# Kernel optimization log

Hardware: AMD Instinct MI355X
Metric: run time of the kernel (lower is better)

Reference implementation:

```python
import jax, jax.numpy as jnp
import numpy as np

B, T, C, H, R = 4, 2048, 1024, 16, 64
D = C // H  # head_dim = 64
ALPHA = 0.7  # init_alpha; alpha_proj is None so c_proj also uses 0.7


def _harmonic_linear(x, U, V):
    # W = U @ diag(s) @ V with harmonic decay s_k = (k+1)^{-alpha}; y = x @ W^T
    s = (jnp.arange(R, dtype=x.dtype) + 1.0) ** (-ALPHA)
    return ((x @ V.T) * s) @ U.T


def setup_inputs() -> dict:
    key = jax.random.key(0)
    ks = jax.random.split(key, 9)
    p = lambda k, shape: 0.02 * jax.random.normal(k, shape, dtype=jnp.float32)
    return {
        "x": jax.random.normal(ks[0], (B, T, C), dtype=jnp.float32),
        "q_U": p(ks[1], (C, R)), "q_V": p(ks[2], (R, C)),
        "k_U": p(ks[3], (C, R)), "k_V": p(ks[4], (R, C)),
        "v_U": p(ks[5], (C, R)), "v_V": p(ks[6], (R, C)),
        "c_U": p(ks[7], (C, R)), "c_V": p(ks[8], (R, C)),
    }


def reference(x, q_U, q_V, k_U, k_V, v_U, v_V, c_U, c_V):
    # projections -> [B, H, T, D]
    def split_heads(t):
        return t.reshape(B, T, H, D).transpose(0, 2, 1, 3)

    q = split_heads(_harmonic_linear(x, q_U, q_V))
    k = split_heads(_harmonic_linear(x, k_U, k_V))
    v = split_heads(_harmonic_linear(x, v_U, v_V))

    scale = 1.0 / np.sqrt(D).astype(np.float32)
    att = jnp.einsum("bhqd,bhkd->bhqk", q, k) * scale  # [B,H,T,T]
    causal = jnp.tril(jnp.ones((T, T), dtype=bool))
    att = jnp.where(causal[None, None], att, jnp.finfo(att.dtype).min)
    att = jax.nn.softmax(att, axis=-1)  # dropout p=0.0 -> identity

    y = jnp.einsum("bhqk,bhkd->bhqd", att, v)  # [B,H,T,D]
    y = y.transpose(0, 2, 1, 3).reshape(B, T, C)
    return _harmonic_linear(y, c_U, c_V)
```

## Files before the change

### kernel.cpp

```cpp
#include <hip/hip_runtime.h>
#include <hip/hip_bf16.h>
#include <math.h>


#define NB 4
#define NT 2048
#define NC 1024
#define NH 16
#define NR 64
#define ND 64
#define NM (NB * NT)

typedef __attribute__((ext_vector_type(8))) short short8;
typedef __attribute__((ext_vector_type(4))) short short4v;
typedef __attribute__((ext_vector_type(4))) float f32x4;
typedef __attribute__((ext_vector_type(4))) float float4v;
typedef __attribute__((ext_vector_type(4))) int int4v;

__device__ __forceinline__ short f2bf(float f) {
    union { __hip_bfloat16 h; short s; } u;
    u.h = __float2bfloat16(f);
    return u.s;
}
__device__ __forceinline__ float bf2f(short s) {
    union { short s; __hip_bfloat16 h; } u;
    u.s = s;
    return __bfloat162float(u.h);
}
__device__ __forceinline__ f32x4 MFMA(short8 a, short8 b, f32x4 c) {
    return __builtin_amdgcn_mfma_f32_16x16x32_bf16(a, b, c, 0, 0, 0);
}
__device__ __forceinline__ float exp2_(float x) {
#if __has_builtin(__builtin_amdgcn_exp2f)
    return __builtin_amdgcn_exp2f(x);
#else
    return exp2f(x);
#endif
}

typedef const __attribute__((address_space(1))) unsigned int* gas_ptr;
typedef __attribute__((address_space(3))) unsigned int* las_ptr;
__device__ __forceinline__ void gll16(const void* g, void* l) {
    __builtin_amdgcn_global_load_lds((gas_ptr)g, (las_ptr)l, 16, 0, 0);
}

__global__ __launch_bounds__(256) void k_prep(const float* __restrict__ qV, const float* __restrict__ kV,
                                              const float* __restrict__ vV, const float* __restrict__ cV,
                                              const float* __restrict__ qU, const float* __restrict__ kU,
                                              const float* __restrict__ vU, const float* __restrict__ cU,
                                              short* __restrict__ Whi, short* __restrict__ Wlo) {
    const int idx = blockIdx.x * 256 + threadIdx.x;
    const int mat = idx >> 13;
    const int f = idx & 8191;
    const int l = f & 63;
    const int rest = f >> 6;
    const float* src;
    switch (mat) {
        case 0: src = qV; break;
        case 1: src = kV; break;
        case 2: src = vV; break;
        case 3: src = cV; break;
        case 4: src = qU; break;
        case 5: src = kU; break;
        case 6: src = vU; break;
        default: src = cU; break;
    }
    int row, col, stride;
    if (mat < 4) {
        const int s = rest & 31, nt = rest >> 5;
        row = nt * 16 + (l & 15);
        col = s * 32 + (l >> 4) * 8;
        stride = NC;
    } else {
        const int ks = rest & 1, tn = rest >> 1;
        row = tn * 16 + (l & 15);
        col = ks * 32 + (l >> 4) * 8;
        stride = NR;
    }
    float sc = 1.0f;
    if (mat < 4) sc = powf((float)(row + 1), -0.7f);
    if (mat == 4) sc = 0.125f * 1.44269504088896f;
    const float* p = src + (size_t)row * stride + col;
    const float4v a = *(const float4v*)p;
    const float4v b = *(const float4v*)(p + 4);
    float v[8] = {a[0], a[1], a[2], a[3], b[0], b[1], b[2], b[3]};
    short* oh = Whi + (size_t)mat * 65536 + (size_t)f * 8;
    short* ol = Wlo + (size_t)mat * 65536 + (size_t)f * 8;
    short4v h0, h1, l0, l1;
#pragma unroll
    for (int j = 0; j < 8; j++) {
        const float fv = v[j] * sc;
        const short h = f2bf(fv);
        const short lo = f2bf(fv - bf2f(h));
        if (j < 4) { h0[j] = h; l0[j] = lo; } else { h1[j - 4] = h; l1[j - 4] = lo; }
    }
    *(short4v*)oh = h0;
    *(short4v*)(oh + 4) = h1;
    *(short4v*)ol = l0;
    *(short4v*)(ol + 4) = l1;
}

__global__ __launch_bounds__(512, 2) void k_qkv(const float* __restrict__ X,
                                                const short* __restrict__ Whi, const short* __restrict__ Wlo,
                                                short* __restrict__ qb, short* __restrict__ kb,
                                                short* __restrict__ vtb) {
    __shared__ __align__(16) char Xl[2][16384];
    __shared__ __align__(16) short Thi[32 * 200];
    __shared__ __align__(16) short Tlov[32 * 72];
    const int tid = threadIdx.x;
    const int w = tid >> 6, l = tid & 63;
    const int lr = l & 15, lk = l >> 4;
    const int g = w & 3, mg = w >> 2;
    const int mb = blockIdx.x * 32;

    auto stageX = [&](int buf, int win) {
#pragma unroll
        for (int q = 0; q < 2; q++) {
            const int r = q * 16 + w * 2 + (l >> 5);
            const int c = l & 31;
            const int sc16 = c ^ (r & 15);
            const float* gp = X + (size_t)(mb + r) * NC + win * 128 + sc16 * 4;
            gll16(gp, (char*)Xl[buf] + q * 8192 + w * 1024);
        }
    };

    const short* Wqk_f = (g < 2) ? Whi : (Whi + 65536);
    const int tA = ((g & 1) * 2) * 32;
    const int tB = tA + 32;
    const int tV = g * 32;
    const short* vfh = Whi + 2 * 65536;
    const short* vfl = Wlo + 2 * 65536;

    f32x4 a0 = 0.0f, a1 = 0.0f, av = 0.0f;
    const int xrow = (mg * 16 + lr) * 512;
    stageX(0, 0);
    for (int win = 0; win < 8; ++win) {
        const int buf = win & 1;
        __syncthreads();
        if (win < 7) stageX(buf ^ 1, win + 1);
        const char* XB = Xl[buf];
#pragma unroll
        for (int kk = 0; kk < 4; ++kk) {
            const int cb = kk * 8 + lk * 2;
            const float4v xa = *(const float4v*)(XB + xrow + ((cb ^ lr) << 4));
            const float4v xb = *(const float4v*)(XB + xrow + (((cb + 1) ^ lr) << 4));
            float xv[8] = {xa[0], xa[1], xa[2], xa[3], xb[0], xb[1], xb[2], xb[3]};
            short8 xh, xl8;
#pragma unroll
            for (int jj = 0; jj < 8; jj++) {
                const short h = f2bf(xv[jj]);
                xh[jj] = h;
                xl8[jj] = f2bf(xv[jj] - bf2f(h));
            }
            const int s = win * 4 + kk;
            const short8 wa = *(const short8*)(Wqk_f + (size_t)((tA + s) * 64 + l) * 8);
            const short8 wb = *(const short8*)(Wqk_f + (size_t)((tB + s) * 64 + l) * 8);
            const short8 wvh = *(const short8*)(vfh + (size_t)((tV + s) * 64 + l) * 8);
            const short8 wvl = *(const short8*)(vfl + (size_t)((tV + s) * 64 + l) * 8);
            a0 = MFMA(xh, wa, a0);
            a1 = MFMA(xh, wb, a1);
            av = MFMA(xh, wvh, av);
            av = MFMA(xh, wvl, av);
            av = MFMA(xl8, wvh, av);
        }
    }
    {
        const int p = g >> 1;
        const int colA = p * 64 + (g & 1) * 32 + lr;
        const int colB = colA + 16;
        const int colV = 128 + g * 16 + lr;
#pragma unroll
        for (int i = 0; i < 4; i++) {
            const int row = mg * 16 + lk * 4 + i;
            Thi[row * 200 + colA] = f2bf(a0[i]);
            Thi[row * 200 + colB] = f2bf(a1[i]);
            const short hv = f2bf(av[i]);
            Thi[row * 200 + colV] = hv;
            Tlov[row * 72 + g * 16 + lr] = f2bf(av[i] - bf2f(hv));
        }
    }
    __syncthreads();
    const short* qUf = Whi + 4 * 65536;
    const short* kUf = Whi + 5 * 65536;
    const short* vUfh = Whi + 6 * 65536;
    const short* vUfl = Wlo + 6 * 65536;
    short8 tf[2][3][2];
    short8 tfl[2][2];
#pragma unroll
    for (int m2 = 0; m2 < 2; m2++) {
        const int trow = m2 * 16 + lr;
#pragma unroll
        for (int ks = 0; ks < 2; ks++) {
#pragma unroll
            for (int p = 0; p < 3; p++)
                tf[m2][p][ks] = *(const short8*)(Thi + trow * 200 + p * 64 + ks * 32 + lk * 8);
            tfl[m2][ks] = *(const short8*)(Tlov + trow * 72 + ks * 32 + lk * 8);
        }
    }
    const int bb = mb >> 11, mt = mb & (NT - 1);
#pragma unroll 2
    for (int nt = 0; nt < 8; nt++) {
        const int tn = w * 8 + nt;
        short8 uq[2], uk[2], uvh[2], uvl[2];
#pragma unroll
        for (int ks = 0; ks < 2; ks++) {
            const size_t off2 = (size_t)((tn * 2 + ks) * 64 + l) * 8;
            uq[ks] = *(const short8*)(qUf + off2);
            uk[ks] = *(const short8*)(kUf + off2);
            uvh[ks] = *(const short8*)(vUfh + off2);
            uvl[ks] = *(const short8*)(vUfl + off2);
        }
#pragma unroll
        for (int m2 = 0; m2 < 2; m2++) {
            f32x4 aq = 0.0f, ak = 0.0f, avv = 0.0f;
#pragma unroll
            for (int ks = 0; ks < 2; ks++) {
                aq = MFMA(uq[ks], tf[m2][0][ks], aq);
                ak = MFMA(uk[ks], tf[m2][1][ks], ak);
                avv = MFMA(tf[m2][2][ks], uvh[ks], avv);
                avv = MFMA(tf[m2][2][ks], uvl[ks], avv);
                avv = MFMA(tfl[m2][ks], uvh[ks], avv);
            }
            const int tt = mt + m2 * 16 + lr;
            const int nq = tn * 16 + lk * 4;
            const int hhq = nq >> 6, ddq = nq & 63;
            short4v pq, pk;
#pragma unroll
            for (int i = 0; i < 4; i++) { pq[i] = f2bf(aq[i]); pk[i] = f2bf(ak[i]); }
            *(short4v*)(qb + ((size_t)(bb * NH + hhq) * NT + tt) * ND + ddq) = pq;
            *(short4v*)(kb + ((size_t)(bb * NH + hhq) * NT + tt) * ND + ddq) = pk;
            const int n = tn * 16 + lr;
            const int hhv = n >> 6, ddv = n & 63;
            const int tv = mt + m2 * 16 + lk * 4;
            short4v pv;
#pragma unroll
            for (int i = 0; i < 4; i++) pv[i] = f2bf(avv[i]);
            *(short4v*)(vtb + ((size_t)(bb * NH + hhv) * ND + ddv) * NT + tv) = pv;
        }
    }
}

__global__ __launch_bounds__(512, 2) void k_cout(const short* __restrict__ Yb,
                                                 const short* __restrict__ Whi, const short* __restrict__ Wlo,
                                                 float* __restrict__ Out) {
    __shared__ __align__(16) char Yl[2][16384];
    __shared__ __align__(16) short tyhi[32 * 72];
    __shared__ __align__(16) short tylo[32 * 72];
    const int tid = threadIdx.x;
    const int w = tid >> 6, l = tid & 63;
    const int lr = l & 15, lk = l >> 4;
    const int g = w & 3, mg = w >> 2;
    const int mb = blockIdx.x * 32;
    const short* cVfh = Whi + 3 * 65536;
    const short* cVfl = Wlo + 3 * 65536;
    const short* cUfh = Whi + 7 * 65536;
    const short* cUfl = Wlo + 7 * 65536;

    auto stageY = [&](int buf, int win) {
#pragma unroll
        for (int q = 0; q < 2; q++) {
            const int r = q * 16 + w * 2 + (l >> 5);
            const int c = l & 31;
            const int sc16 = c ^ (r & 15);
            const short* gp = Yb + (size_t)(mb + r) * NC + win * 256 + sc16 * 8;
            gll16(gp, (char*)Yl[buf] + q * 8192 + w * 1024);
        }
    };

    const int tV = g * 32;
    f32x4 acc = 0.0f;
    const int xrow = (mg * 16 + lr) * 512;
    stageY(0, 0);
    for (int win = 0; win < 4; ++win) {
        const int buf = win & 1;
        __syncthreads();
        if (win < 3) stageY(buf ^ 1, win + 1);
        const char* YB = Yl[buf];
#pragma unroll
        for (int kk = 0; kk < 8; ++kk) {
            const short8 ah = *(const short8*)(YB + xrow + ((((kk * 4 + lk)) ^ lr) << 4));
            const int s = win * 8 + kk;
            const short8 wh = *(const short8*)(cVfh + (size_t)((tV + s) * 64 + l) * 8);
            const short8 wl = *(const short8*)(cVfl + (size_t)((tV + s) * 64 + l) * 8);
            acc = MFMA(ah, wh, acc);
            acc = MFMA(ah, wl, acc);
        }
    }
#pragma unroll
    for (int i = 0; i < 4; i++) {
        const int row = mg * 16 + lk * 4 + i;
        const short h = f2bf(acc[i]);
        tyhi[row * 72 + g * 16 + lr] = h;
        tylo[row * 72 + g * 16 + lr] = f2bf(acc[i] - bf2f(h));
    }
    __syncthreads();
    short8 th[2][2], tl[2][2];
#pragma unroll
    for (int m2 = 0; m2 < 2; m2++) {
        const int trow = m2 * 16 + lr;
#pragma unroll
        for (int ks = 0; ks < 2; ks++) {
            th[m2][ks] = *(const short8*)(tyhi + trow * 72 + ks * 32 + lk * 8);
            tl[m2][ks] = *(const short8*)(tylo + trow * 72 + ks * 32 + lk * 8);
        }
    }
#pragma unroll 2
    for (int nt = 0; nt < 8; nt++) {
        const int tn = w * 8 + nt;
        short8 uh[2], ul[2];
#pragma unroll
        for (int ks = 0; ks < 2; ks++) {
            const size_t off2 = (size_t)((tn * 2 + ks) * 64 + l) * 8;
            uh[ks] = *(const short8*)(cUfh + off2);
            ul[ks] = *(const short8*)(cUfl + off2);
        }
#pragma unroll
        for (int m2 = 0; m2 < 2; m2++) {
            f32x4 a = 0.0f;
#pragma unroll
            for (int ks = 0; ks < 2; ks++) {
                a = MFMA(uh[ks], th[m2][ks], a);
                a = MFMA(ul[ks], th[m2][ks], a);
                a = MFMA(uh[ks], tl[m2][ks], a);
            }
            const int mm = mb + m2 * 16 + lr;
            const int n = tn * 16 + lk * 4;
            *(float4v*)(Out + (size_t)mm * NC + n) = *(float4v*)&a;
        }
    }
}

__device__ __forceinline__ short8 lds_frag(const short* base, int row, int cb) {
    return *(const short8*)((const char*)base + (((row << 7) + cb) ^ ((row & 7) << 4)));
}

__global__ __launch_bounds__(256, 2) void k_attn(const short* __restrict__ Qm,
                                                 const short* __restrict__ Km,
                                                 const short* __restrict__ Vt,
                                                 short* __restrict__ Y) {
    __shared__ __align__(16) short Kl[2][64 * 64];
    __shared__ __align__(16) short Vl[2][64 * 64];
    __shared__ __align__(16) short Pl[8 * 1024];
    const int tid = threadIdx.x;
    const int w = tid >> 6, l = tid & 63;
    const int lr = l & 15, lk = l >> 4;
    const int lin = blockIdx.y * 8 + blockIdx.x;
    const int nl = (lin & 7) * 64 + (lin >> 3);
    const int j = nl & 7;
    const int bh = nl >> 3;
    const int ntile = 32 - 2 * j;
    const int qA0 = 128 * j + w * 32;
    const int qB0 = (1920 - 128 * j) + w * 32;
    const int diagA = 2 * j + (w >> 1);
    const int diagB = 30 - 2 * j + (w >> 1);

    const short* Kb = Km + (size_t)bh * NT * ND;
    const short* Vb = Vt + (size_t)bh * ND * NT;

    short8 qfA[2][2], qfB[2][2];
#pragma unroll
    for (int f = 0; f < 2; f++) {
#pragma unroll
        for (int ks = 0; ks < 2; ks++) {
            qfA[f][ks] = *(const short8*)(Qm + ((size_t)bh * NT + qA0 + f * 16 + lr) * ND + ks * 32 + lk * 8);
            qfB[f][ks] = *(const short8*)(Qm + ((size_t)bh * NT + qB0 + f * 16 + lr) * ND + ks * 32 + lk * 8);
        }
    }

    const int grow8 = w * 8 + (l >> 3);
    const int gcolb = (((l & 7) ^ ((l >> 3) & 7)) << 4);
    auto stage = [&](int buf, int kv0) {
        const char* kp = (const char*)Kb + (((size_t)(kv0 + grow8)) << 7) + gcolb;
        const char* vp = (const char*)Vb + (size_t)grow8 * (NT * 2) + kv0 * 2 + gcolb;
        char* kl = (char*)Kl[buf] + w * 1024;
        char* vl = (char*)Vl[buf] + w * 1024;
        gll16(kp, kl);
        gll16(kp + (32 << 7), kl + 4096);
        gll16(vp, vl);
        gll16(vp + (size_t)32 * NT * 2, vl + 4096);
    };

    f32x4 lsA[2], lsB[2];
    f32x4 oA[2][4], oB[2][4];
#pragma unroll
    for (int f = 0; f < 2; f++) {
        lsA[f] = 0.0f;
        lsB[f] = 0.0f;
#pragma unroll
        for (int dt = 0; dt < 4; dt++) { oA[f][dt] = 0.0f; oB[f][dt] = 0.0f; }
    }

    auto computeG = [&](const short8 (&qf)[2][2], f32x4 (&ls)[2], f32x4 (&o)[2][4],
                        const short* KlB, const short* VlB, bool diag) {
        f32x4 sa[2][4];
#pragma unroll
        for (int f = 0; f < 2; f++)
#pragma unroll
            for (int nt = 0; nt < 4; nt++) sa[f][nt] = -16.0f;
        __builtin_amdgcn_s_setprio(1);
#pragma unroll
        for (int ks = 0; ks < 2; ks++) {
#pragma unroll
            for (int nt = 0; nt < 4; nt++) {
                const short8 kf = lds_frag(KlB, nt * 16 + lr, ks * 64 + lk * 16);
                sa[0][nt] = MFMA(kf, qf[0][ks], sa[0][nt]);
                sa[1][nt] = MFMA(kf, qf[1][ks], sa[1][nt]);
            }
        }
        __builtin_amdgcn_s_setprio(0);
        if (diag) {
#pragma unroll
            for (int f = 0; f < 2; f++) {
                const int qrel = (w & 1) * 32 + f * 16 + lr;
#pragma unroll
                for (int nt = 0; nt < 4; nt++) {
                    const int kvb = nt * 16 + lk * 4;
#pragma unroll
                    for (int i = 0; i < 4; i++)
                        if (kvb + i > qrel) sa[f][nt][i] = -1e30f;
                }
            }
        }
#pragma unroll
        for (int f = 0; f < 2; f++) {
            char* plbf = (char*)Pl + w * 4096 + f * 2048;
#pragma unroll
            for (int nt = 0; nt < 4; nt++) {
                f32x4 sv;
#pragma unroll
                for (int i = 0; i < 4; i++) sv[i] = exp2_(sa[f][nt][i]);
                ls[f] += sv;
                short4v pk;
#pragma unroll
                for (int i = 0; i < 4; i++) pk[i] = f2bf(sv[i]);
                *(short4v*)(plbf + (((lr << 7) + ((nt * 16 + lk * 4) << 1)) ^ ((lr & 7) << 4))) = pk;
            }
        }
        short8 pb[2][2];
#pragma unroll
        for (int f = 0; f < 2; f++) {
            const char* plbf = (const char*)Pl + w * 4096 + f * 2048;
            pb[f][0] = *(const short8*)(plbf + (((lr << 7) + ((lk * 8) << 1)) ^ ((lr & 7) << 4)));
            pb[f][1] = *(const short8*)(plbf + (((lr << 7) + ((32 + lk * 8) << 1)) ^ ((lr & 7) << 4)));
        }
        __builtin_amdgcn_s_setprio(1);
#pragma unroll
        for (int ks = 0; ks < 2; ks++) {
#pragma unroll
            for (int dt = 0; dt < 4; dt++) {
                const short8 vf = lds_frag(VlB, dt * 16 + lr, ks * 64 + lk * 16);
                o[0][dt] = MFMA(vf, pb[0][ks], o[0][dt]);
                o[1][dt] = MFMA(vf, pb[1][ks], o[1][dt]);
            }
        }
        __builtin_amdgcn_s_setprio(0);
    };

    stage(0, 0);
    for (int it = 0; it < ntile; ++it) {
        const int buf = it & 1;
        __syncthreads();
        if (it + 1 < ntile) stage(buf ^ 1, (it + 1) * 64);
        const short* KlB = Kl[buf];
        const short* VlB = Vl[buf];
        if (it <= diagA) computeG(qfA, lsA, oA, KlB, VlB, it == diagA);
        if (it <= diagB) computeG(qfB, lsB, oB, KlB, VlB, it == diagB);
    }

    const int b = bh >> 4, h = bh & 15;
#pragma unroll
    for (int f = 0; f < 2; f++) {
        float lA = (lsA[f][0] + lsA[f][1]) + (lsA[f][2] + lsA[f][3]);
        float lB = (lsB[f][0] + lsB[f][1]) + (lsB[f][2] + lsB[f][3]);
        lA += __shfl_xor(lA, 16);
        lA += __shfl_xor(lA, 32);
        lB += __shfl_xor(lB, 16);
        lB += __shfl_xor(lB, 32);
        const float invA = 1.0f / lA, invB = 1.0f / lB;
        short* ypA = Y + ((size_t)b * NT + (qA0 + f * 16 + lr)) * NC + h * ND;
        short* ypB = Y + ((size_t)b * NT + (qB0 + f * 16 + lr)) * NC + h * ND;
#pragma unroll
        for (int dt = 0; dt < 4; dt++) {
            short4v ya, yb2;
#pragma unroll
            for (int i = 0; i < 4; i++) {
                ya[i] = f2bf(oA[f][dt][i] * invA);
                yb2[i] = f2bf(oB[f][dt][i] * invB);
            }
            *(short4v*)(ypA + dt * 16 + lk * 4) = ya;
            *(short4v*)(ypB + dt * 16 + lk * 4) = yb2;
        }
    }
}

extern "C" void kernel_launch(void* const* d_in, const int* in_sizes, int n_in,
                              void* d_out, int out_size, void* d_ws, size_t ws_size,
                              hipStream_t stream) {
    const float* x = (const float*)d_in[0];
    const float* qU = (const float*)d_in[1];
    const float* qV = (const float*)d_in[2];
    const float* kU = (const float*)d_in[3];
    const float* kV = (const float*)d_in[4];
    const float* vU = (const float*)d_in[5];
    const float* vV = (const float*)d_in[6];
    const float* cU = (const float*)d_in[7];
    const float* cV = (const float*)d_in[8];
    float* out = (float*)d_out;

    char* ws = (char*)d_ws;
    size_t off = 0;
    auto take = [&](size_t bytes) {
        char* p = ws + off;
        off += (bytes + 255) & ~(size_t)255;
        return p;
    };
    short* Whi = (short*)take(8 * 65536 * 2);
    short* Wlo = (short*)take(8 * 65536 * 2);
    short* qb = (short*)take((size_t)NM * NC * 2);
    short* kb = (short*)take((size_t)NM * NC * 2);
    short* vtb = (short*)take((size_t)NM * NC * 2);
    short* yb = (short*)take((size_t)NM * NC * 2);

    k_prep<<<256, 256, 0, stream>>>(qV, kV, vV, cV, qU, kU, vU, cU, Whi, Wlo);
    k_qkv<<<256, 512, 0, stream>>>(x, Whi, Wlo, qb, kb, vtb);
    k_attn<<<dim3(8, NB * NH), 256, 0, stream>>>(qb, kb, vtb, yb);
    k_cout<<<256, 512, 0, stream>>>(yb, Whi, Wlo, out);
}
```

Measured before the change: 117.8 us.

## Stage 128-key KV tiles and share K/V fragments across both query groups

Doubles the shared-memory K/V stage from 64 to 128 keys per barrier, halving the number of __syncthreads in the attention loop. The QK/softmax and PV stages are split so K and V fragments are read from LDS once per sub-tile into registers and reused by both query groups A and B, instead of being reloaded for each group. In exchange, LDS use per block roughly doubles and register pressure rises from the held K/V fragment arrays, which may reduce occupancy.

```diff
diff --git a/kernel.cpp b/kernel.cpp
--- a/kernel.cpp
+++ b/kernel.cpp
@@ -338,8 +338,8 @@
                                                  const short* __restrict__ Km,
                                                  const short* __restrict__ Vt,
                                                  short* __restrict__ Y) {
-    __shared__ __align__(16) short Kl[2][64 * 64];
-    __shared__ __align__(16) short Vl[2][64 * 64];
+    __shared__ __align__(16) short Kl[2][8192];
+    __shared__ __align__(16) short Vl[2][8192];
     __shared__ __align__(16) short Pl[8 * 1024];
     const int tid = threadIdx.x;
     const int w = tid >> 6, l = tid & 63;
@@ -349,6 +349,7 @@
     const int j = nl & 7;
     const int bh = nl >> 3;
     const int ntile = 32 - 2 * j;
+    const int np = 16 - j;
     const int qA0 = 128 * j + w * 32;
     const int qB0 = (1920 - 128 * j) + w * 32;
     const int diagA = 2 * j + (w >> 1);
@@ -369,15 +370,20 @@
 
     const int grow8 = w * 8 + (l >> 3);
     const int gcolb = (((l & 7) ^ ((l >> 3) & 7)) << 4);
-    auto stage = [&](int buf, int kv0) {
-        const char* kp = (const char*)Kb + (((size_t)(kv0 + grow8)) << 7) + gcolb;
-        const char* vp = (const char*)Vb + (size_t)grow8 * (NT * 2) + kv0 * 2 + gcolb;
+    auto stage2 = [&](int buf, int kv0) {
         char* kl = (char*)Kl[buf] + w * 1024;
         char* vl = (char*)Vl[buf] + w * 1024;
-        gll16(kp, kl);
-        gll16(kp + (32 << 7), kl + 4096);
-        gll16(vp, vl);
-        gll16(vp + (size_t)32 * NT * 2, vl + 4096);
+#pragma unroll
+        for (int c = 0; c < 4; ++c) {
+            const char* kp = (const char*)Kb + (((size_t)(kv0 + c * 32 + grow8)) << 7) + gcolb;
+            gll16(kp, kl + c * 4096);
+        }
+#pragma unroll
+        for (int c = 0; c < 4; ++c) {
+            const int tt = c >> 1, dh = c & 1;
+            const char* vp = (const char*)Vb + (size_t)(dh * 32 + grow8) * (NT * 2) + (kv0 + tt * 64) * 2 + gcolb;
+            gll16(vp, vl + tt * 8192 + dh * 4096);
+        }
     };
 
     f32x4 lsA[2], lsB[2];
@@ -390,8 +396,8 @@
         for (int dt = 0; dt < 4; dt++) { oA[f][dt] = 0.0f; oB[f][dt] = 0.0f; }
     }
 
-    auto computeG = [&](const short8 (&qf)[2][2], f32x4 (&ls)[2], f32x4 (&o)[2][4],
-                        const short* KlB, const short* VlB, bool diag) {
+    auto qk_sm = [&](const short8 (&qf)[2][2], const short8 (&kfr)[2][4],
+                     f32x4 (&ls)[2], short8 (&pb)[2][2], bool diag) {
         f32x4 sa[2][4];
 #pragma unroll
         for (int f = 0; f < 2; f++)
@@ -402,9 +408,8 @@
         for (int ks = 0; ks < 2; ks++) {
 #pragma unroll
             for (int nt = 0; nt < 4; nt++) {
-                const short8 kf = lds_frag(KlB, nt * 16 + lr, ks * 64 + lk * 16);
-                sa[0][nt] = MFMA(kf, qf[0][ks], sa[0][nt]);
-                sa[1][nt] = MFMA(kf, qf[1][ks], sa[1][nt]);
+                sa[0][nt] = MFMA(kfr[ks][nt], qf[0][ks], sa[0][nt]);
+                sa[1][nt] = MFMA(kfr[ks][nt], qf[1][ks], sa[1][nt]);
             }
         }
         __builtin_amdgcn_s_setprio(0);
@@ -436,35 +441,56 @@
                 *(short4v*)(plbf + (((lr << 7) + ((nt * 16 + lk * 4) << 1)) ^ ((lr & 7) << 4))) = pk;
             }
         }
-        short8 pb[2][2];
 #pragma unroll
         for (int f = 0; f < 2; f++) {
             const char* plbf = (const char*)Pl + w * 4096 + f * 2048;
             pb[f][0] = *(const short8*)(plbf + (((lr << 7) + ((lk * 8) << 1)) ^ ((lr & 7) << 4)));
             pb[f][1] = *(const short8*)(plbf + (((lr << 7) + ((32 + lk * 8) << 1)) ^ ((lr & 7) << 4)));
         }
+    };
+    auto pv = [&](const short8 (&pb)[2][2], const short8 (&vfr)[2][4], f32x4 (&o)[2][4]) {
         __builtin_amdgcn_s_setprio(1);
 #pragma unroll
         for (int ks = 0; ks < 2; ks++) {
 #pragma unroll
             for (int dt = 0; dt < 4; dt++) {
-                const short8 vf = lds_frag(VlB, dt * 16 + lr, ks * 64 + lk * 16);
-                o[0][dt] = MFMA(vf, pb[0][ks], o[0][dt]);
-                o[1][dt] = MFMA(vf, pb[1][ks], o[1][dt]);
+                o[0][dt] = MFMA(vfr[ks][dt], pb[0][ks], o[0][dt]);
+                o[1][dt] = MFMA(vfr[ks][dt], pb[1][ks], o[1][dt]);
             }
         }
         __builtin_amdgcn_s_setprio(0);
     };
 
-    stage(0, 0);
-    for (int it = 0; it < ntile; ++it) {
-        const int buf = it & 1;
+    stage2(0, 0);
+    for (int p = 0; p < np; ++p) {
+        const int buf = p & 1;
         __syncthreads();
-        if (it + 1 < ntile) stage(buf ^ 1, (it + 1) * 64);
-        const short* KlB = Kl[buf];
-        const short* VlB = Vl[buf];
-        if (it <= diagA) computeG(qfA, lsA, oA, KlB, VlB, it == diagA);
-        if (it <= diagB) computeG(qfB, lsB, oB, KlB, VlB, it == diagB);
+        if (p + 1 < np) stage2(buf ^ 1, (p + 1) * 128);
+#pragma unroll
+        for (int t = 0; t < 2; ++t) {
+            const int it = p * 2 + t;
+            const short* KlB = Kl[buf] + t * 4096;
+            const short* VlB = Vl[buf] + t * 4096;
+            const bool aA = (it <= diagA);
+            const bool aB = (it <= diagB);
+            short8 kfr[2][4];
+#pragma unroll
+            for (int ks = 0; ks < 2; ks++)
+#pragma unroll
+                for (int nt = 0; nt < 4; nt++)
+                    kfr[ks][nt] = lds_frag(KlB, nt * 16 + lr, ks * 64 + lk * 16);
+            short8 pbA[2][2], pbB[2][2];
+            if (aA) qk_sm(qfA, kfr, lsA, pbA, it == diagA);
+            if (aB) qk_sm(qfB, kfr, lsB, pbB, it == diagB);
+            short8 vfr[2][4];
+#pragma unroll
+            for (int ks = 0; ks < 2; ks++)
+#pragma unroll
+                for (int dt = 0; dt < 4; dt++)
+                    vfr[ks][dt] = lds_frag(VlB, dt * 16 + lr, ks * 64 + lk * 16);
+            if (aA) pv(pbA, vfr, oA);
+            if (aB) pv(pbB, vfr, oB);
+        }
     }
 
     const int b = bh >> 4, h = bh & 15;
```

After: 117.8 us. No clear change (-0.0%).

## Split paired causal query tiles into separate blocks, largest first, with higher occupancy

Applied to the files above, without the earlier changes.

The attention kernel no longer pairs a short and a long causal query tile in one block. Each block now handles a single 128-row query tile, so the grid doubles. Blocks are ordered longest-first for load balance, and launch bounds rise to 4 blocks per CU by halving the P scratch in LDS. K and V fragments are also hoisted into registers before the MFMA loops. The cost is that K/V tiles are staged from global memory separately by each block instead of being shared by two query groups, and more blocks have uneven lengths.

```diff
diff --git a/kernel.cpp b/kernel.cpp
--- a/kernel.cpp
+++ b/kernel.cpp
@@ -334,37 +334,33 @@
     return *(const short8*)((const char*)base + (((row << 7) + cb) ^ ((row & 7) << 4)));
 }
 
-__global__ __launch_bounds__(256, 2) void k_attn(const short* __restrict__ Qm,
+__global__ __launch_bounds__(256, 4) void k_attn(const short* __restrict__ Qm,
                                                  const short* __restrict__ Km,
                                                  const short* __restrict__ Vt,
                                                  short* __restrict__ Y) {
-    __shared__ __align__(16) short Kl[2][64 * 64];
-    __shared__ __align__(16) short Vl[2][64 * 64];
-    __shared__ __align__(16) short Pl[8 * 1024];
+    __shared__ __align__(16) short Kl[2][4096];
+    __shared__ __align__(16) short Vl[2][4096];
+    __shared__ __align__(16) short Pl[4][1024];
     const int tid = threadIdx.x;
     const int w = tid >> 6, l = tid & 63;
     const int lr = l & 15, lk = l >> 4;
-    const int lin = blockIdx.y * 8 + blockIdx.x;
-    const int nl = (lin & 7) * 64 + (lin >> 3);
-    const int j = nl & 7;
-    const int bh = nl >> 3;
-    const int ntile = 32 - 2 * j;
-    const int qA0 = 128 * j + w * 32;
-    const int qB0 = (1920 - 128 * j) + w * 32;
-    const int diagA = 2 * j + (w >> 1);
-    const int diagB = 30 - 2 * j + (w >> 1);
+    const int lin = blockIdx.y * 16 + blockIdx.x;
+    const int nl = (lin & 7) * 128 + (lin >> 3);
+    const int bh = nl >> 4;
+    const int j = 15 - (nl & 15);
+    const int np = 2 * j + 2;
+    const int diagw = 2 * j + (w >> 1);
+    const int q0 = 128 * j + 32 * w;
 
     const short* Kb = Km + (size_t)bh * NT * ND;
     const short* Vb = Vt + (size_t)bh * ND * NT;
 
-    short8 qfA[2][2], qfB[2][2];
+    short8 qf[2][2];
 #pragma unroll
     for (int f = 0; f < 2; f++) {
 #pragma unroll
-        for (int ks = 0; ks < 2; ks++) {
-            qfA[f][ks] = *(const short8*)(Qm + ((size_t)bh * NT + qA0 + f * 16 + lr) * ND + ks * 32 + lk * 8);
-            qfB[f][ks] = *(const short8*)(Qm + ((size_t)bh * NT + qB0 + f * 16 + lr) * ND + ks * 32 + lk * 8);
-        }
+        for (int ks = 0; ks < 2; ks++)
+            qf[f][ks] = *(const short8*)(Qm + ((size_t)bh * NT + q0 + f * 16 + lr) * ND + ks * 32 + lk * 8);
     }
 
     const int grow8 = w * 8 + (l >> 3);
@@ -380,115 +376,100 @@
         gll16(vp + (size_t)32 * NT * 2, vl + 4096);
     };
 
-    f32x4 lsA[2], lsB[2];
-    f32x4 oA[2][4], oB[2][4];
+    f32x4 ls[2];
+    f32x4 o[2][4];
 #pragma unroll
     for (int f = 0; f < 2; f++) {
-        lsA[f] = 0.0f;
-        lsB[f] = 0.0f;
-#pragma unroll
-        for (int dt = 0; dt < 4; dt++) { oA[f][dt] = 0.0f; oB[f][dt] = 0.0f; }
-    }
-
-    auto computeG = [&](const short8 (&qf)[2][2], f32x4 (&ls)[2], f32x4 (&o)[2][4],
-                        const short* KlB, const short* VlB, bool diag) {
-        f32x4 sa[2][4];
-#pragma unroll
-        for (int f = 0; f < 2; f++)
-#pragma unroll
-            for (int nt = 0; nt < 4; nt++) sa[f][nt] = -16.0f;
-        __builtin_amdgcn_s_setprio(1);
-#pragma unroll
-        for (int ks = 0; ks < 2; ks++) {
-#pragma unroll
-            for (int nt = 0; nt < 4; nt++) {
-                const short8 kf = lds_frag(KlB, nt * 16 + lr, ks * 64 + lk * 16);
-                sa[0][nt] = MFMA(kf, qf[0][ks], sa[0][nt]);
-                sa[1][nt] = MFMA(kf, qf[1][ks], sa[1][nt]);
-            }
-        }
-        __builtin_amdgcn_s_setprio(0);
-        if (diag) {
-#pragma unroll
-            for (int f = 0; f < 2; f++) {
+        ls[f] = 0.0f;
+#pragma unroll
+        for (int dt = 0; dt < 4; dt++) o[f][dt] = 0.0f;
+    }
+
+    char* plw = (char*)Pl[w];
+
+    stage(0, 0);
+    for (int it = 0; it < np; ++it) {
+        const int buf = it & 1;
+        __syncthreads();
+        if (it + 1 < np) stage(buf ^ 1, (it + 1) * 64);
+        if (it > diagw) continue;
+        const short* KlB = Kl[buf];
+        const short* VlB = Vl[buf];
+        const bool diag = (it == diagw);
+        short8 kfr[2][4];
+#pragma unroll
+        for (int ks = 0; ks < 2; ks++)
+#pragma unroll
+            for (int nt = 0; nt < 4; nt++)
+                kfr[ks][nt] = lds_frag(KlB, nt * 16 + lr, ks * 64 + lk * 16);
+        short8 pb[2][2];
+#pragma unroll
+        for (int f = 0; f < 2; f++) {
+            f32x4 sa[4];
+#pragma unroll
+            for (int nt = 0; nt < 4; nt++) sa[nt] = -16.0f;
+            __builtin_amdgcn_s_setprio(1);
+#pragma unroll
+            for (int ks = 0; ks < 2; ks++)
+#pragma unroll
+                for (int nt = 0; nt < 4; nt++)
+                    sa[nt] = MFMA(kfr[ks][nt], qf[f][ks], sa[nt]);
+            __builtin_amdgcn_s_setprio(0);
+            if (diag) {
                 const int qrel = (w & 1) * 32 + f * 16 + lr;
 #pragma unroll
                 for (int nt = 0; nt < 4; nt++) {
                     const int kvb = nt * 16 + lk * 4;
 #pragma unroll
                     for (int i = 0; i < 4; i++)
-                        if (kvb + i > qrel) sa[f][nt][i] = -1e30f;
+                        if (kvb + i > qrel) sa[nt][i] = -1e30f;
                 }
             }
-        }
-#pragma unroll
-        for (int f = 0; f < 2; f++) {
-            char* plbf = (char*)Pl + w * 4096 + f * 2048;
 #pragma unroll
             for (int nt = 0; nt < 4; nt++) {
                 f32x4 sv;
 #pragma unroll
-                for (int i = 0; i < 4; i++) sv[i] = exp2_(sa[f][nt][i]);
+                for (int i = 0; i < 4; i++) sv[i] = exp2_(sa[nt][i]);
                 ls[f] += sv;
                 short4v pk;
 #pragma unroll
                 for (int i = 0; i < 4; i++) pk[i] = f2bf(sv[i]);
-                *(short4v*)(plbf + (((lr << 7) + ((nt * 16 + lk * 4) << 1)) ^ ((lr & 7) << 4))) = pk;
+                *(short4v*)(plw + (((lr << 7) + ((nt * 16 + lk * 4) << 1)) ^ ((lr & 7) << 4))) = pk;
             }
-        }
-        short8 pb[2][2];
-#pragma unroll
-        for (int f = 0; f < 2; f++) {
-            const char* plbf = (const char*)Pl + w * 4096 + f * 2048;
-            pb[f][0] = *(const short8*)(plbf + (((lr << 7) + ((lk * 8) << 1)) ^ ((lr & 7) << 4)));
-            pb[f][1] = *(const short8*)(plbf + (((lr << 7) + ((32 + lk * 8) << 1)) ^ ((lr & 7) << 4)));
-        }
+            pb[f][0] = *(const short8*)(plw + (((lr << 7) + ((lk * 8) << 1)) ^ ((lr & 7) << 4)));
+            pb[f][1] = *(const short8*)(plw + (((lr << 7) + ((32 + lk * 8) << 1)) ^ ((lr & 7) << 4)));
+        }
+        short8 vfr[2][4];
+#pragma unroll
+        for (int ks = 0; ks < 2; ks++)
+#pragma unroll
+            for (int dt = 0; dt < 4; dt++)
+                vfr[ks][dt] = lds_frag(VlB, dt * 16 + lr, ks * 64 + lk * 16);
         __builtin_amdgcn_s_setprio(1);
 #pragma unroll
-        for (int ks = 0; ks < 2; ks++) {
+        for (int ks = 0; ks < 2; ks++)
 #pragma unroll
             for (int dt = 0; dt < 4; dt++) {
-                const short8 vf = lds_frag(VlB, dt * 16 + lr, ks * 64 + lk * 16);
-                o[0][dt] = MFMA(vf, pb[0][ks], o[0][dt]);
-                o[1][dt] = MFMA(vf, pb[1][ks], o[1][dt]);
+                o[0][dt] = MFMA(vfr[ks][dt], pb[0][ks], o[0][dt]);
+                o[1][dt] = MFMA(vfr[ks][dt], pb[1][ks], o[1][dt]);
             }
-        }
         __builtin_amdgcn_s_setprio(0);
-    };
-
-    stage(0, 0);
-    for (int it = 0; it < ntile; ++it) {
-        const int buf = it & 1;
-        __syncthreads();
-        if (it + 1 < ntile) stage(buf ^ 1, (it + 1) * 64);
-        const short* KlB = Kl[buf];
-        const short* VlB = Vl[buf];
-        if (it <= diagA) computeG(qfA, lsA, oA, KlB, VlB, it == diagA);
-        if (it <= diagB) computeG(qfB, lsB, oB, KlB, VlB, it == diagB);
     }
 
     const int b = bh >> 4, h = bh & 15;
 #pragma unroll
     for (int f = 0; f < 2; f++) {
-        float lA = (lsA[f][0] + lsA[f][1]) + (lsA[f][2] + lsA[f][3]);
-        float lB = (lsB[f][0] + lsB[f][1]) + (lsB[f][2] + lsB[f][3]);
-        lA += __shfl_xor(lA, 16);
-        lA += __shfl_xor(lA, 32);
-        lB += __shfl_xor(lB, 16);
-        lB += __shfl_xor(lB, 32);
-        const float invA = 1.0f / lA, invB = 1.0f / lB;
-        short* ypA = Y + ((size_t)b * NT + (qA0 + f * 16 + lr)) * NC + h * ND;
-        short* ypB = Y + ((size_t)b * NT + (qB0 + f * 16 + lr)) * NC + h * ND;
+        float lsum = (ls[f][0] + ls[f][1]) + (ls[f][2] + ls[f][3]);
+        lsum += __shfl_xor(lsum, 16);
+        lsum += __shfl_xor(lsum, 32);
+        const float inv = 1.0f / lsum;
+        short* yp = Y + ((size_t)b * NT + (q0 + f * 16 + lr)) * NC + h * ND;
 #pragma unroll
         for (int dt = 0; dt < 4; dt++) {
-            short4v ya, yb2;
-#pragma unroll
-            for (int i = 0; i < 4; i++) {
-                ya[i] = f2bf(oA[f][dt][i] * invA);
-                yb2[i] = f2bf(oB[f][dt][i] * invB);
-            }
-            *(short4v*)(ypA + dt * 16 + lk * 4) = ya;
-            *(short4v*)(ypB + dt * 16 + lk * 4) = yb2;
+            short4v ya;
+#pragma unroll
+            for (int i = 0; i < 4; i++) ya[i] = f2bf(o[f][dt][i] * inv);
+            *(short4v*)(yp + dt * 16 + lk * 4) = ya;
         }
     }
 }
@@ -523,6 +504,6 @@
 
     k_prep<<<256, 256, 0, stream>>>(qV, kV, vV, cV, qU, kU, vU, cU, Whi, Wlo);
     k_qkv<<<256, 512, 0, stream>>>(x, Whi, Wlo, qb, kb, vtb);
-    k_attn<<<dim3(8, NB * NH), 256, 0, stream>>>(qb, kb, vtb, yb);
+    k_attn<<<dim3(16, NB * NH), 256, 0, stream>>>(qb, kb, vtb, yb);
     k_cout<<<256, 512, 0, stream>>>(yb, Whi, Wlo, out);
 }
```

New measurement: 195.9 us. 1.66x slower.
